# Optimization experiments

Hardware: AMD Instinct MI355X
Metric: run time of the kernel (lower is better)

## Reference

```python
import jax, jax.numpy as jnp
import numpy as np

B, S, D = 4, 4096, 64

def setup_inputs() -> dict:
    key = jax.random.key(0)
    k1, k2, k3 = jax.random.split(key, 3)
    inputs = jax.random.normal(k1, (B, S, D), dtype=jnp.float32)
    rotation = jax.random.normal(k2, (D, D), dtype=jnp.float32)
    entangle = jax.random.normal(k3, (D, D), dtype=jnp.float32)
    return {"inputs": inputs, "rotation": rotation, "entangle": entangle}

def reference(inputs, rotation, entangle):
    # query/key projections: [B,S,D] @ [D,D] -> [B,S,D]
    query = jnp.einsum('bsd,de->bse', inputs, rotation)
    key = jnp.einsum('bsd,de->bse', inputs, entangle)
    scale = 1.0 / jnp.sqrt(jnp.float32(inputs.shape[-1]))
    # scores: [B,S,S] softmax over last axis
    scores = jax.nn.softmax(jnp.einsum('bqd,bkd->bqk', query, key) * scale, axis=-1)
    # values are the raw inputs (no value projection)
    return jnp.einsum('bqk,bkd->bqd', scores, inputs)
```

## Files before the change

kernel.cpp:

```cpp
#include <hip/hip_runtime.h>
#include <hip/hip_fp16.h>

#define BB 4
#define SS 4096
#define DD 64
#define NSPLIT 4
#define KT_PER (SS / 64 / NSPLIT)

typedef _Float16 half8 __attribute__((ext_vector_type(8)));
typedef _Float16 half4 __attribute__((ext_vector_type(4)));
typedef __fp16 fp16x2 __attribute__((ext_vector_type(2)));
typedef float floatx4 __attribute__((ext_vector_type(4)));

__global__ __launch_bounds__(256) void proj_kernel(
    const float* __restrict__ X, const float* __restrict__ R, const float* __restrict__ E,
    _Float16* __restrict__ Qhi, _Float16* __restrict__ Qlo,
    _Float16* __restrict__ Khi, _Float16* __restrict__ Klo,
    _Float16* __restrict__ Vt)
{
    __shared__ float Rs[64][64];
    __shared__ float Es[64][64];
    __shared__ float Xs[16][68];
    int t = threadIdx.x;
    long rowbase = (long)blockIdx.x * 16;

    for (int j = 0; j < 4; ++j) {
        int idx = j * 256 + t;
        int r = idx >> 4;
        int c = (idx & 15) * 4;
        *(float4*)&Rs[r][c] = ((const float4*)R)[idx];
        *(float4*)&Es[r][c] = ((const float4*)E)[idx];
    }
    *(float4*)&Xs[t >> 4][(t & 15) * 4] = ((const float4*)(X + rowbase * 64))[t];
    __syncthreads();

    int row = t >> 4;
    int c0 = (t & 15) * 4;
    float q[4] = {0.f, 0.f, 0.f, 0.f}, k[4] = {0.f, 0.f, 0.f, 0.f};
#pragma unroll 4
    for (int d = 0; d < 64; ++d) {
        float x = Xs[row][d];
        float4 rv = *(const float4*)&Rs[d][c0];
        float4 ev = *(const float4*)&Es[d][c0];
        q[0] = fmaf(x, rv.x, q[0]); q[1] = fmaf(x, rv.y, q[1]);
        q[2] = fmaf(x, rv.z, q[2]); q[3] = fmaf(x, rv.w, q[3]);
        k[0] = fmaf(x, ev.x, k[0]); k[1] = fmaf(x, ev.y, k[1]);
        k[2] = fmaf(x, ev.z, k[2]); k[3] = fmaf(x, ev.w, k[3]);
    }
    long gq = (rowbase + row) * 64 + c0;
    half4 qh, ql, kh, kl;
    for (int j = 0; j < 4; ++j) {
        _Float16 h = (_Float16)q[j];
        qh[j] = h; ql[j] = (_Float16)(q[j] - (float)h);
        h = (_Float16)k[j];
        kh[j] = h; kl[j] = (_Float16)(k[j] - (float)h);
    }
    *(half4*)(Qhi + gq) = qh; *(half4*)(Qlo + gq) = ql;
    *(half4*)(Khi + gq) = kh; *(half4*)(Klo + gq) = kl;

    int d = t >> 2;
    int si = (t & 3) * 4;
    int b = (int)(rowbase >> 12);
    int sbase = (int)(rowbase & 4095);
    half4 v;
    for (int j = 0; j < 4; ++j) v[j] = (_Float16)Xs[si + j][d];
    *(half4*)(Vt + ((long)(b * 64 + d)) * SS + sbase + si) = v;
}

#define L2E 1.44269504088896340736f
#define PD 72

__global__ __launch_bounds__(256, 4) void attn_partial(
    const _Float16* __restrict__ Qhi, const _Float16* __restrict__ Qlo,
    const _Float16* __restrict__ Khi, const _Float16* __restrict__ Klo,
    const _Float16* __restrict__ Vt,
    float* __restrict__ Op, float* __restrict__ Mp, float* __restrict__ Lp)
{
    __shared__ _Float16 Ksh[64][PD];
    __shared__ _Float16 Ksl[64][PD];
    __shared__ _Float16 Vs[64][PD];
    __shared__ _Float16 Ps[4][16][PD];

    int t = threadIdx.x;
    int wave = t >> 6;
    int lane = t & 63;
    int l15 = lane & 15;
    int quad = lane >> 4;
    int split = blockIdx.y;
    int b = blockIdx.z;
    int q0 = blockIdx.x * 64 + wave * 16;

    long qrow = ((long)b * SS + q0 + l15) * DD;
    half8 qa0h = *(const half8*)(Qhi + qrow + quad * 8);
    half8 qa1h = *(const half8*)(Qhi + qrow + 32 + quad * 8);
    half8 qa0l = *(const half8*)(Qlo + qrow + quad * 8);
    half8 qa1l = *(const half8*)(Qlo + qrow + 32 + quad * 8);

    floatx4 o[4];
    for (int i = 0; i < 4; ++i) o[i] = (floatx4){0.f, 0.f, 0.f, 0.f};
    float m_q = -1e30f;
    float l_q = 0.f;

    const float scale = 0.125f * L2E;

    int rr = t >> 2;
    int cc = (t & 3) * 16;
    long kbase = ((long)b * SS + rr) * DD + cc;
    long vbase = ((long)b * 64 + rr) * SS + cc;

    int kt = split * KT_PER;
    uint4 rh0, rh1, rl0, rl1, rv0, rv1;
    {
        const uint4* khsrc = (const uint4*)(Khi + kbase + (long)kt * 64 * DD);
        rh0 = khsrc[0]; rh1 = khsrc[1];
        const uint4* klsrc = (const uint4*)(Klo + kbase + (long)kt * 64 * DD);
        rl0 = klsrc[0]; rl1 = klsrc[1];
        const uint4* vsrc = (const uint4*)(Vt + vbase + kt * 64);
        rv0 = vsrc[0]; rv1 = vsrc[1];
    }

    for (int i = 0; i < KT_PER; ++i) {
        if (i > 0) __syncthreads();
        {
            uint4* khdst = (uint4*)&Ksh[rr][cc];
            khdst[0] = rh0; khdst[1] = rh1;
            uint4* kldst = (uint4*)&Ksl[rr][cc];
            kldst[0] = rl0; kldst[1] = rl1;
            uint4* vdst = (uint4*)&Vs[rr][cc];
            vdst[0] = rv0; vdst[1] = rv1;
        }
        __syncthreads();

        int ktn = (i + 1 < KT_PER) ? (kt + 1) : kt;
        {
            const uint4* khsrc = (const uint4*)(Khi + kbase + (long)ktn * 64 * DD);
            rh0 = khsrc[0]; rh1 = khsrc[1];
            const uint4* klsrc = (const uint4*)(Klo + kbase + (long)ktn * 64 * DD);
            rl0 = klsrc[0]; rl1 = klsrc[1];
            const uint4* vsrc = (const uint4*)(Vt + vbase + ktn * 64);
            rv0 = vsrc[0]; rv1 = vsrc[1];
        }
        kt = ktn;

        floatx4 s[4];
        for (int ct = 0; ct < 4; ++ct) {
            floatx4 acc = {0.f, 0.f, 0.f, 0.f};
            half8 ka0h = *(const half8*)&Ksh[ct * 16 + l15][quad * 8];
            half8 ka1h = *(const half8*)&Ksh[ct * 16 + l15][32 + quad * 8];
            half8 ka0l = *(const half8*)&Ksl[ct * 16 + l15][quad * 8];
            half8 ka1l = *(const half8*)&Ksl[ct * 16 + l15][32 + quad * 8];
            acc = __builtin_amdgcn_mfma_f32_16x16x32_f16(ka0h, qa0h, acc, 0, 0, 0);
            acc = __builtin_amdgcn_mfma_f32_16x16x32_f16(ka1h, qa1h, acc, 0, 0, 0);
            acc = __builtin_amdgcn_mfma_f32_16x16x32_f16(ka0h, qa0l, acc, 0, 0, 0);
            acc = __builtin_amdgcn_mfma_f32_16x16x32_f16(ka1h, qa1l, acc, 0, 0, 0);
            acc = __builtin_amdgcn_mfma_f32_16x16x32_f16(ka0l, qa0h, acc, 0, 0, 0);
            acc = __builtin_amdgcn_mfma_f32_16x16x32_f16(ka1l, qa1h, acc, 0, 0, 0);
            s[ct] = acc;
        }

        float mt = s[0][0];
        for (int ct = 0; ct < 4; ++ct)
            for (int r = 0; r < 4; ++r)
                mt = fmaxf(mt, s[ct][r]);
        mt = fmaxf(mt, __shfl_xor(mt, 16));
        mt = fmaxf(mt, __shfl_xor(mt, 32));
        mt *= scale;
        float mn = fmaxf(m_q, mt);
        float alpha = exp2f(m_q - mn);
        m_q = mn;

        float rs = 0.f;
        for (int ct = 0; ct < 4; ++ct) {
            float p0 = exp2f(s[ct][0] * scale - mn);
            float p1 = exp2f(s[ct][1] * scale - mn);
            float p2 = exp2f(s[ct][2] * scale - mn);
            float p3 = exp2f(s[ct][3] * scale - mn);
            rs += (p0 + p1) + (p2 + p3);
            union { fp16x2 h2[2]; half4 h4; } u;
            u.h2[0] = __builtin_amdgcn_cvt_pkrtz(p0, p1);
            u.h2[1] = __builtin_amdgcn_cvt_pkrtz(p2, p3);
            *(half4*)&Ps[wave][l15][ct * 16 + quad * 4] = u.h4;
        }
        rs += __shfl_xor(rs, 16);
        rs += __shfl_xor(rs, 32);
        l_q = l_q * alpha + rs;

        for (int r = 0; r < 4; ++r) {
            float a = __shfl(alpha, quad * 4 + r);
            o[0][r] *= a; o[1][r] *= a; o[2][r] *= a; o[3][r] *= a;
        }

        for (int h = 0; h < 2; ++h) {
            half8 pa = *(const half8*)&Ps[wave][l15][h * 32 + quad * 8];
            for (int dt = 0; dt < 4; ++dt) {
                half8 vb = *(const half8*)&Vs[dt * 16 + l15][h * 32 + quad * 8];
                o[dt] = __builtin_amdgcn_mfma_f32_16x16x32_f16(pa, vb, o[dt], 0, 0, 0);
            }
        }
    }

    long pbase = ((long)b * NSPLIT + split) * SS;
    for (int r = 0; r < 4; ++r) {
        int q = q0 + quad * 4 + r;
        long orow = (pbase + q) * DD;
        for (int dt = 0; dt < 4; ++dt)
            Op[orow + dt * 16 + l15] = o[dt][r];
    }
    if (quad == 0) {
        Mp[pbase + q0 + l15] = m_q;
        Lp[pbase + q0 + l15] = l_q;
    }
}

__global__ __launch_bounds__(256) void combine_kernel(
    const float* __restrict__ Op, const float* __restrict__ Mp,
    const float* __restrict__ Lp, float* __restrict__ Out)
{
    int t = threadIdx.x;
    int qi = t >> 4;
    int d4 = (t & 15) * 4;
    long gq = (long)blockIdx.x * 16 + qi;
    int b = (int)(gq >> 12);
    int s = (int)(gq & 4095);

    float m = -1e30f;
    for (int i = 0; i < NSPLIT; ++i)
        m = fmaxf(m, Mp[((long)b * NSPLIT + i) * SS + s]);
    float l = 0.f;
    float4 o = {0.f, 0.f, 0.f, 0.f};
    for (int i = 0; i < NSPLIT; ++i) {
        long pb = ((long)b * NSPLIT + i) * SS + s;
        float a = exp2f(Mp[pb] - m);
        l = fmaf(Lp[pb], a, l);
        float4 oi = *(const float4*)(Op + pb * DD + d4);
        o.x = fmaf(oi.x, a, o.x); o.y = fmaf(oi.y, a, o.y);
        o.z = fmaf(oi.z, a, o.z); o.w = fmaf(oi.w, a, o.w);
    }
    float inv = 1.f / l;
    float4 r = {o.x * inv, o.y * inv, o.z * inv, o.w * inv};
    *(float4*)(Out + gq * DD + d4) = r;
}

extern "C" void kernel_launch(void* const* d_in, const int* in_sizes, int n_in,
                              void* d_out, int out_size, void* d_ws, size_t ws_size,
                              hipStream_t stream) {
    const float* X = (const float*)d_in[0];
    const float* R = (const float*)d_in[1];
    const float* E = (const float*)d_in[2];
    float* Out = (float*)d_out;

    const size_t N = (size_t)BB * SS * DD;
    _Float16* Qhi = (_Float16*)d_ws;
    _Float16* Qlo = Qhi + N;
    _Float16* Khi = Qlo + N;
    _Float16* Klo = Khi + N;
    _Float16* Vt  = Klo + N;
    float* Op = (float*)(Vt + N);
    float* Mp = Op + (size_t)BB * NSPLIT * SS * DD;
    float* Lp = Mp + (size_t)BB * NSPLIT * SS;

    proj_kernel<<<dim3(BB * SS / 16), 256, 0, stream>>>(X, R, E, Qhi, Qlo, Khi, Klo, Vt);
    attn_partial<<<dim3(SS / 64, NSPLIT, BB), 256, 0, stream>>>(Qhi, Qlo, Khi, Klo, Vt, Op, Mp, Lp);
    combine_kernel<<<dim3(BB * SS / 16), 256, 0, stream>>>(Op, Mp, Lp, Out);
}
```

Before: 119.8 us.

## Give each attention wave two query tiles and batch projection rows per block

The attention kernel now runs with 128 threads (2 waves), and each wave handles 32 query rows as two 16-row tiles. Each K/V fragment read from shared memory therefore feeds twice as many MFMAs, which cuts LDS traffic per unit of compute. K/V tile loads are redistributed over fewer threads with more loads each. The projection kernel now processes 64 rows per block instead of 16, so the R/E weight loads are amortised over more rows and the Vt stores are wider. Costs are higher register pressure, fewer threads per block, and fewer projection blocks.

```diff
diff --git a/kernel.cpp b/kernel.cpp
--- a/kernel.cpp
+++ b/kernel.cpp
@@ -20,57 +20,69 @@
 {
     __shared__ float Rs[64][64];
     __shared__ float Es[64][64];
-    __shared__ float Xs[16][68];
+    __shared__ float Xs[64][68];
     int t = threadIdx.x;
-    long rowbase = (long)blockIdx.x * 16;
-
+    long rowbase = (long)blockIdx.x * 64;
+
+    const float4* Xg = (const float4*)(X + rowbase * 64);
     for (int j = 0; j < 4; ++j) {
         int idx = j * 256 + t;
         int r = idx >> 4;
         int c = (idx & 15) * 4;
         *(float4*)&Rs[r][c] = ((const float4*)R)[idx];
         *(float4*)&Es[r][c] = ((const float4*)E)[idx];
-    }
-    *(float4*)&Xs[t >> 4][(t & 15) * 4] = ((const float4*)(X + rowbase * 64))[t];
+        *(float4*)&Xs[r][c] = Xg[idx];
+    }
     __syncthreads();
 
-    int row = t >> 4;
+    int rg = t >> 4;
     int c0 = (t & 15) * 4;
-    float q[4] = {0.f, 0.f, 0.f, 0.f}, k[4] = {0.f, 0.f, 0.f, 0.f};
+    float q[4][4], k[4][4];
+    for (int i = 0; i < 4; ++i)
+        for (int j = 0; j < 4; ++j) { q[i][j] = 0.f; k[i][j] = 0.f; }
 #pragma unroll 4
     for (int d = 0; d < 64; ++d) {
-        float x = Xs[row][d];
         float4 rv = *(const float4*)&Rs[d][c0];
         float4 ev = *(const float4*)&Es[d][c0];
-        q[0] = fmaf(x, rv.x, q[0]); q[1] = fmaf(x, rv.y, q[1]);
-        q[2] = fmaf(x, rv.z, q[2]); q[3] = fmaf(x, rv.w, q[3]);
-        k[0] = fmaf(x, ev.x, k[0]); k[1] = fmaf(x, ev.y, k[1]);
-        k[2] = fmaf(x, ev.z, k[2]); k[3] = fmaf(x, ev.w, k[3]);
-    }
-    long gq = (rowbase + row) * 64 + c0;
-    half4 qh, ql, kh, kl;
-    for (int j = 0; j < 4; ++j) {
-        _Float16 h = (_Float16)q[j];
-        qh[j] = h; ql[j] = (_Float16)(q[j] - (float)h);
-        h = (_Float16)k[j];
-        kh[j] = h; kl[j] = (_Float16)(k[j] - (float)h);
-    }
-    *(half4*)(Qhi + gq) = qh; *(half4*)(Qlo + gq) = ql;
-    *(half4*)(Khi + gq) = kh; *(half4*)(Klo + gq) = kl;
+        for (int i = 0; i < 4; ++i) {
+            float x = Xs[rg * 4 + i][d];
+            q[i][0] = fmaf(x, rv.x, q[i][0]); q[i][1] = fmaf(x, rv.y, q[i][1]);
+            q[i][2] = fmaf(x, rv.z, q[i][2]); q[i][3] = fmaf(x, rv.w, q[i][3]);
+            k[i][0] = fmaf(x, ev.x, k[i][0]); k[i][1] = fmaf(x, ev.y, k[i][1]);
+            k[i][2] = fmaf(x, ev.z, k[i][2]); k[i][3] = fmaf(x, ev.w, k[i][3]);
+        }
+    }
+    for (int i = 0; i < 4; ++i) {
+        long gq = (rowbase + rg * 4 + i) * 64 + c0;
+        half4 qh, ql, kh, kl;
+        for (int j = 0; j < 4; ++j) {
+            _Float16 h = (_Float16)q[i][j];
+            qh[j] = h; ql[j] = (_Float16)(q[i][j] - (float)h);
+            h = (_Float16)k[i][j];
+            kh[j] = h; kl[j] = (_Float16)(k[i][j] - (float)h);
+        }
+        *(half4*)(Qhi + gq) = qh; *(half4*)(Qlo + gq) = ql;
+        *(half4*)(Khi + gq) = kh; *(half4*)(Klo + gq) = kl;
+    }
 
     int d = t >> 2;
-    int si = (t & 3) * 4;
+    int si = (t & 3) * 16;
     int b = (int)(rowbase >> 12);
     int sbase = (int)(rowbase & 4095);
-    half4 v;
-    for (int j = 0; j < 4; ++j) v[j] = (_Float16)Xs[si + j][d];
-    *(half4*)(Vt + ((long)(b * 64 + d)) * SS + sbase + si) = v;
+    half8 v0, v1;
+    for (int j = 0; j < 8; ++j) {
+        v0[j] = (_Float16)Xs[si + j][d];
+        v1[j] = (_Float16)Xs[si + 8 + j][d];
+    }
+    _Float16* vp = Vt + ((long)(b * 64 + d)) * SS + sbase + si;
+    *(half8*)vp = v0;
+    *(half8*)(vp + 8) = v1;
 }
 
 #define L2E 1.44269504088896340736f
 #define PD 72
 
-__global__ __launch_bounds__(256, 4) void attn_partial(
+__global__ __launch_bounds__(128, 2) void attn_partial(
     const _Float16* __restrict__ Qhi, const _Float16* __restrict__ Qlo,
     const _Float16* __restrict__ Khi, const _Float16* __restrict__ Klo,
     const _Float16* __restrict__ Vt,
@@ -79,7 +91,7 @@
     __shared__ _Float16 Ksh[64][PD];
     __shared__ _Float16 Ksl[64][PD];
     __shared__ _Float16 Vs[64][PD];
-    __shared__ _Float16 Ps[4][16][PD];
+    __shared__ _Float16 Ps[2][32][PD];
 
     int t = threadIdx.x;
     int wave = t >> 6;
@@ -88,127 +100,144 @@
     int quad = lane >> 4;
     int split = blockIdx.y;
     int b = blockIdx.z;
-    int q0 = blockIdx.x * 64 + wave * 16;
-
-    long qrow = ((long)b * SS + q0 + l15) * DD;
-    half8 qa0h = *(const half8*)(Qhi + qrow + quad * 8);
-    half8 qa1h = *(const half8*)(Qhi + qrow + 32 + quad * 8);
-    half8 qa0l = *(const half8*)(Qlo + qrow + quad * 8);
-    half8 qa1l = *(const half8*)(Qlo + qrow + 32 + quad * 8);
-
-    floatx4 o[4];
-    for (int i = 0; i < 4; ++i) o[i] = (floatx4){0.f, 0.f, 0.f, 0.f};
-    float m_q = -1e30f;
-    float l_q = 0.f;
+    int q0 = blockIdx.x * 64 + wave * 32;
+
+    half8 qah[2][2], qal[2][2];
+    for (int qh = 0; qh < 2; ++qh) {
+        long qrow = ((long)b * SS + q0 + qh * 16 + l15) * DD;
+        qah[qh][0] = *(const half8*)(Qhi + qrow + quad * 8);
+        qah[qh][1] = *(const half8*)(Qhi + qrow + 32 + quad * 8);
+        qal[qh][0] = *(const half8*)(Qlo + qrow + quad * 8);
+        qal[qh][1] = *(const half8*)(Qlo + qrow + 32 + quad * 8);
+    }
+
+    floatx4 o[2][4];
+    for (int qh = 0; qh < 2; ++qh)
+        for (int i = 0; i < 4; ++i) o[qh][i] = (floatx4){0.f, 0.f, 0.f, 0.f};
+    float m_q[2] = {-1e30f, -1e30f};
+    float l_q[2] = {0.f, 0.f};
 
     const float scale = 0.125f * L2E;
 
-    int rr = t >> 2;
-    int cc = (t & 3) * 16;
-    long kbase = ((long)b * SS + rr) * DD + cc;
-    long vbase = ((long)b * 64 + rr) * SS + cc;
-
+    int erow = t >> 3;
+    int eel = (t & 7) * 8;
+    long ktilebase = ((long)b * SS) * DD;
     int kt = split * KT_PER;
-    uint4 rh0, rh1, rl0, rl1, rv0, rv1;
+
+    uint4 rh[4], rl[4], rv[4];
     {
-        const uint4* khsrc = (const uint4*)(Khi + kbase + (long)kt * 64 * DD);
-        rh0 = khsrc[0]; rh1 = khsrc[1];
-        const uint4* klsrc = (const uint4*)(Klo + kbase + (long)kt * 64 * DD);
-        rl0 = klsrc[0]; rl1 = klsrc[1];
-        const uint4* vsrc = (const uint4*)(Vt + vbase + kt * 64);
-        rv0 = vsrc[0]; rv1 = vsrc[1];
+        const uint4* khsrc = (const uint4*)(Khi + ktilebase + (long)kt * 64 * DD) + t;
+        const uint4* klsrc = (const uint4*)(Klo + ktilebase + (long)kt * 64 * DD) + t;
+        for (int j = 0; j < 4; ++j) {
+            rh[j] = khsrc[j * 128];
+            rl[j] = klsrc[j * 128];
+            int d = j * 16 + erow;
+            rv[j] = *(const uint4*)(Vt + ((long)(b * 64 + d)) * SS + kt * 64 + eel);
+        }
     }
 
     for (int i = 0; i < KT_PER; ++i) {
         if (i > 0) __syncthreads();
-        {
-            uint4* khdst = (uint4*)&Ksh[rr][cc];
-            khdst[0] = rh0; khdst[1] = rh1;
-            uint4* kldst = (uint4*)&Ksl[rr][cc];
-            kldst[0] = rl0; kldst[1] = rl1;
-            uint4* vdst = (uint4*)&Vs[rr][cc];
-            vdst[0] = rv0; vdst[1] = rv1;
+        for (int j = 0; j < 4; ++j) {
+            int rr = j * 16 + erow;
+            *(uint4*)&Ksh[rr][eel] = rh[j];
+            *(uint4*)&Ksl[rr][eel] = rl[j];
+            *(uint4*)&Vs[rr][eel] = rv[j];
         }
         __syncthreads();
 
         int ktn = (i + 1 < KT_PER) ? (kt + 1) : kt;
         {
-            const uint4* khsrc = (const uint4*)(Khi + kbase + (long)ktn * 64 * DD);
-            rh0 = khsrc[0]; rh1 = khsrc[1];
-            const uint4* klsrc = (const uint4*)(Klo + kbase + (long)ktn * 64 * DD);
-            rl0 = klsrc[0]; rl1 = klsrc[1];
-            const uint4* vsrc = (const uint4*)(Vt + vbase + ktn * 64);
-            rv0 = vsrc[0]; rv1 = vsrc[1];
+            const uint4* khsrc = (const uint4*)(Khi + ktilebase + (long)ktn * 64 * DD) + t;
+            const uint4* klsrc = (const uint4*)(Klo + ktilebase + (long)ktn * 64 * DD) + t;
+            for (int j = 0; j < 4; ++j) {
+                rh[j] = khsrc[j * 128];
+                rl[j] = klsrc[j * 128];
+                int d = j * 16 + erow;
+                rv[j] = *(const uint4*)(Vt + ((long)(b * 64 + d)) * SS + ktn * 64 + eel);
+            }
         }
         kt = ktn;
 
-        floatx4 s[4];
+        floatx4 s[2][4];
         for (int ct = 0; ct < 4; ++ct) {
-            floatx4 acc = {0.f, 0.f, 0.f, 0.f};
             half8 ka0h = *(const half8*)&Ksh[ct * 16 + l15][quad * 8];
             half8 ka1h = *(const half8*)&Ksh[ct * 16 + l15][32 + quad * 8];
             half8 ka0l = *(const half8*)&Ksl[ct * 16 + l15][quad * 8];
             half8 ka1l = *(const half8*)&Ksl[ct * 16 + l15][32 + quad * 8];
-            acc = __builtin_amdgcn_mfma_f32_16x16x32_f16(ka0h, qa0h, acc, 0, 0, 0);
-            acc = __builtin_amdgcn_mfma_f32_16x16x32_f16(ka1h, qa1h, acc, 0, 0, 0);
-            acc = __builtin_amdgcn_mfma_f32_16x16x32_f16(ka0h, qa0l, acc, 0, 0, 0);
-            acc = __builtin_amdgcn_mfma_f32_16x16x32_f16(ka1h, qa1l, acc, 0, 0, 0);
-            acc = __builtin_amdgcn_mfma_f32_16x16x32_f16(ka0l, qa0h, acc, 0, 0, 0);
-            acc = __builtin_amdgcn_mfma_f32_16x16x32_f16(ka1l, qa1h, acc, 0, 0, 0);
-            s[ct] = acc;
-        }
-
-        float mt = s[0][0];
-        for (int ct = 0; ct < 4; ++ct)
-            for (int r = 0; r < 4; ++r)
-                mt = fmaxf(mt, s[ct][r]);
-        mt = fmaxf(mt, __shfl_xor(mt, 16));
-        mt = fmaxf(mt, __shfl_xor(mt, 32));
-        mt *= scale;
-        float mn = fmaxf(m_q, mt);
-        float alpha = exp2f(m_q - mn);
-        m_q = mn;
-
-        float rs = 0.f;
-        for (int ct = 0; ct < 4; ++ct) {
-            float p0 = exp2f(s[ct][0] * scale - mn);
-            float p1 = exp2f(s[ct][1] * scale - mn);
-            float p2 = exp2f(s[ct][2] * scale - mn);
-            float p3 = exp2f(s[ct][3] * scale - mn);
-            rs += (p0 + p1) + (p2 + p3);
-            union { fp16x2 h2[2]; half4 h4; } u;
-            u.h2[0] = __builtin_amdgcn_cvt_pkrtz(p0, p1);
-            u.h2[1] = __builtin_amdgcn_cvt_pkrtz(p2, p3);
-            *(half4*)&Ps[wave][l15][ct * 16 + quad * 4] = u.h4;
-        }
-        rs += __shfl_xor(rs, 16);
-        rs += __shfl_xor(rs, 32);
-        l_q = l_q * alpha + rs;
-
-        for (int r = 0; r < 4; ++r) {
-            float a = __shfl(alpha, quad * 4 + r);
-            o[0][r] *= a; o[1][r] *= a; o[2][r] *= a; o[3][r] *= a;
+            for (int qh = 0; qh < 2; ++qh) {
+                floatx4 acc = {0.f, 0.f, 0.f, 0.f};
+                acc = __builtin_amdgcn_mfma_f32_16x16x32_f16(ka0h, qah[qh][0], acc, 0, 0, 0);
+                acc = __builtin_amdgcn_mfma_f32_16x16x32_f16(ka1h, qah[qh][1], acc, 0, 0, 0);
+                acc = __builtin_amdgcn_mfma_f32_16x16x32_f16(ka0h, qal[qh][0], acc, 0, 0, 0);
+                acc = __builtin_amdgcn_mfma_f32_16x16x32_f16(ka1h, qal[qh][1], acc, 0, 0, 0);
+                acc = __builtin_amdgcn_mfma_f32_16x16x32_f16(ka0l, qah[qh][0], acc, 0, 0, 0);
+                acc = __builtin_amdgcn_mfma_f32_16x16x32_f16(ka1l, qah[qh][1], acc, 0, 0, 0);
+                s[qh][ct] = acc;
+            }
+        }
+
+        float alpha[2];
+        for (int qh = 0; qh < 2; ++qh) {
+            float mt = s[qh][0][0];
+            for (int ct = 0; ct < 4; ++ct)
+                for (int r = 0; r < 4; ++r)
+                    mt = fmaxf(mt, s[qh][ct][r]);
+            mt = fmaxf(mt, __shfl_xor(mt, 16));
+            mt = fmaxf(mt, __shfl_xor(mt, 32));
+            mt *= scale;
+            float mn = fmaxf(m_q[qh], mt);
+            alpha[qh] = exp2f(m_q[qh] - mn);
+            m_q[qh] = mn;
+
+            float rs = 0.f;
+            for (int ct = 0; ct < 4; ++ct) {
+                float p0 = exp2f(s[qh][ct][0] * scale - mn);
+                float p1 = exp2f(s[qh][ct][1] * scale - mn);
+                float p2 = exp2f(s[qh][ct][2] * scale - mn);
+                float p3 = exp2f(s[qh][ct][3] * scale - mn);
+                rs += (p0 + p1) + (p2 + p3);
+                union { fp16x2 h2[2]; half4 h4; } u;
+                u.h2[0] = __builtin_amdgcn_cvt_pkrtz(p0, p1);
+                u.h2[1] = __builtin_amdgcn_cvt_pkrtz(p2, p3);
+                *(half4*)&Ps[wave][qh * 16 + l15][ct * 16 + quad * 4] = u.h4;
+            }
+            rs += __shfl_xor(rs, 16);
+            rs += __shfl_xor(rs, 32);
+            l_q[qh] = l_q[qh] * alpha[qh] + rs;
+
+            for (int r = 0; r < 4; ++r) {
+                float a = __shfl(alpha[qh], quad * 4 + r);
+                o[qh][0][r] *= a; o[qh][1][r] *= a;
+                o[qh][2][r] *= a; o[qh][3][r] *= a;
+            }
         }
 
         for (int h = 0; h < 2; ++h) {
-            half8 pa = *(const half8*)&Ps[wave][l15][h * 32 + quad * 8];
+            half8 pa0 = *(const half8*)&Ps[wave][l15][h * 32 + quad * 8];
+            half8 pa1 = *(const half8*)&Ps[wave][16 + l15][h * 32 + quad * 8];
             for (int dt = 0; dt < 4; ++dt) {
                 half8 vb = *(const half8*)&Vs[dt * 16 + l15][h * 32 + quad * 8];
-                o[dt] = __builtin_amdgcn_mfma_f32_16x16x32_f16(pa, vb, o[dt], 0, 0, 0);
+                o[0][dt] = __builtin_amdgcn_mfma_f32_16x16x32_f16(pa0, vb, o[0][dt], 0, 0, 0);
+                o[1][dt] = __builtin_amdgcn_mfma_f32_16x16x32_f16(pa1, vb, o[1][dt], 0, 0, 0);
             }
         }
     }
 
     long pbase = ((long)b * NSPLIT + split) * SS;
-    for (int r = 0; r < 4; ++r) {
-        int q = q0 + quad * 4 + r;
-        long orow = (pbase + q) * DD;
-        for (int dt = 0; dt < 4; ++dt)
-            Op[orow + dt * 16 + l15] = o[dt][r];
+    for (int qh = 0; qh < 2; ++qh) {
+        for (int r = 0; r < 4; ++r) {
+            int q = q0 + qh * 16 + quad * 4 + r;
+            long orow = (pbase + q) * DD;
+            for (int dt = 0; dt < 4; ++dt)
+                Op[orow + dt * 16 + l15] = o[qh][dt][r];
+        }
     }
     if (quad == 0) {
-        Mp[pbase + q0 + l15] = m_q;
-        Lp[pbase + q0 + l15] = l_q;
+        for (int qh = 0; qh < 2; ++qh) {
+            Mp[pbase + q0 + qh * 16 + l15] = m_q[qh];
+            Lp[pbase + q0 + qh * 16 + l15] = l_q[qh];
+        }
     }
 }
 
@@ -259,7 +288,7 @@
     float* Mp = Op + (size_t)BB * NSPLIT * SS * DD;
     float* Lp = Mp + (size_t)BB * NSPLIT * SS;
 
-    proj_kernel<<<dim3(BB * SS / 16), 256, 0, stream>>>(X, R, E, Qhi, Qlo, Khi, Klo, Vt);
-    attn_partial<<<dim3(SS / 64, NSPLIT, BB), 256, 0, stream>>>(Qhi, Qlo, Khi, Klo, Vt, Op, Mp, Lp);
+    proj_kernel<<<dim3(BB * SS / 64), 256, 0, stream>>>(X, R, E, Qhi, Qlo, Khi, Klo, Vt);
+    attn_partial<<<dim3(SS / 64, NSPLIT, BB), 128, 0, stream>>>(Qhi, Qlo, Khi, Klo, Vt, Op, Mp, Lp);
     combine_kernel<<<dim3(BB * SS / 16), 256, 0, stream>>>(Op, Mp, Lp, Out);
 }
```

After: 218.1 us. 1.82x slower.

## Use 2-wave blocks with 32 queries per wave and direct global-to-LDS loads

Applied to the files above, without the earlier changes.

The attention kernel now runs 128-thread blocks in which each wave handles 32 query rows (two 16-row MFMA groups), so every K/V fragment read from LDS is reused across twice as many queries. K and V tiles are copied with global_load_lds into XOR-swizzled, unpadded LDS buffers instead of being staged through registers. The register-prefetch double buffer is removed, so global loads are no longer overlapped with compute. Register pressure per wave also rises.

```diff
diff --git a/kernel.cpp b/kernel.cpp
--- a/kernel.cpp
+++ b/kernel.cpp
@@ -49,6 +49,7 @@
     }
     long gq = (rowbase + row) * 64 + c0;
     half4 qh, ql, kh, kl;
+#pragma unroll
     for (int j = 0; j < 4; ++j) {
         _Float16 h = (_Float16)q[j];
         qh[j] = h; ql[j] = (_Float16)(q[j] - (float)h);
@@ -63,23 +64,29 @@
     int b = (int)(rowbase >> 12);
     int sbase = (int)(rowbase & 4095);
     half4 v;
+#pragma unroll
     for (int j = 0; j < 4; ++j) v[j] = (_Float16)Xs[si + j][d];
     *(half4*)(Vt + ((long)(b * 64 + d)) * SS + sbase + si) = v;
 }
 
 #define L2E 1.44269504088896340736f
-#define PD 72
-
-__global__ __launch_bounds__(256, 4) void attn_partial(
+
+__device__ __forceinline__ void glds16(const _Float16* g, _Float16* l) {
+    __builtin_amdgcn_global_load_lds(
+        (const __attribute__((address_space(1))) unsigned*)g,
+        (__attribute__((address_space(3))) unsigned*)l, 16, 0, 0);
+}
+
+__global__ __launch_bounds__(128, 2) void attn_partial(
     const _Float16* __restrict__ Qhi, const _Float16* __restrict__ Qlo,
     const _Float16* __restrict__ Khi, const _Float16* __restrict__ Klo,
     const _Float16* __restrict__ Vt,
     float* __restrict__ Op, float* __restrict__ Mp, float* __restrict__ Lp)
 {
-    __shared__ _Float16 Ksh[64][PD];
-    __shared__ _Float16 Ksl[64][PD];
-    __shared__ _Float16 Vs[64][PD];
-    __shared__ _Float16 Ps[4][16][PD];
+    __shared__ _Float16 Ksh[64 * 64];
+    __shared__ _Float16 Ksl[64 * 64];
+    __shared__ _Float16 Vs[64 * 64];
+    __shared__ _Float16 Ps[2][32][72];
 
     int t = threadIdx.x;
     int wave = t >> 6;
@@ -88,127 +95,154 @@
     int quad = lane >> 4;
     int split = blockIdx.y;
     int b = blockIdx.z;
-    int q0 = blockIdx.x * 64 + wave * 16;
-
-    long qrow = ((long)b * SS + q0 + l15) * DD;
-    half8 qa0h = *(const half8*)(Qhi + qrow + quad * 8);
-    half8 qa1h = *(const half8*)(Qhi + qrow + 32 + quad * 8);
-    half8 qa0l = *(const half8*)(Qlo + qrow + quad * 8);
-    half8 qa1l = *(const half8*)(Qlo + qrow + 32 + quad * 8);
-
-    floatx4 o[4];
-    for (int i = 0; i < 4; ++i) o[i] = (floatx4){0.f, 0.f, 0.f, 0.f};
-    float m_q = -1e30f;
-    float l_q = 0.f;
+    int q0 = blockIdx.x * 64 + wave * 32;
+
+    half8 qah0, qah1, qbh0, qbh1, qal0, qal1, qbl0, qbl1;
+    {
+        long qrow = ((long)b * SS + q0 + l15) * DD;
+        qah0 = *(const half8*)(Qhi + qrow + quad * 8);
+        qah1 = *(const half8*)(Qhi + qrow + 32 + quad * 8);
+        qal0 = *(const half8*)(Qlo + qrow + quad * 8);
+        qal1 = *(const half8*)(Qlo + qrow + 32 + quad * 8);
+        long qrow2 = qrow + 16 * DD;
+        qbh0 = *(const half8*)(Qhi + qrow2 + quad * 8);
+        qbh1 = *(const half8*)(Qhi + qrow2 + 32 + quad * 8);
+        qbl0 = *(const half8*)(Qlo + qrow2 + quad * 8);
+        qbl1 = *(const half8*)(Qlo + qrow2 + 32 + quad * 8);
+    }
+
+    floatx4 o[2][4];
+#pragma unroll
+    for (int qh = 0; qh < 2; ++qh)
+#pragma unroll
+        for (int i = 0; i < 4; ++i) o[qh][i] = (floatx4){0.f, 0.f, 0.f, 0.f};
+    float m_q[2] = {-1e30f, -1e30f};
+    float l_q[2] = {0.f, 0.f};
 
     const float scale = 0.125f * L2E;
 
-    int rr = t >> 2;
-    int cc = (t & 3) * 16;
-    long kbase = ((long)b * SS + rr) * DD + cc;
-    long vbase = ((long)b * 64 + rr) * SS + cc;
+    int grow = lane >> 3;
+    int gblk = (lane & 7) ^ grow;
+    int rm = l15 & 7;
+    int p0h = ((quad ^ rm) << 3);
 
     int kt = split * KT_PER;
-    uint4 rh0, rh1, rl0, rl1, rv0, rv1;
-    {
-        const uint4* khsrc = (const uint4*)(Khi + kbase + (long)kt * 64 * DD);
-        rh0 = khsrc[0]; rh1 = khsrc[1];
-        const uint4* klsrc = (const uint4*)(Klo + kbase + (long)kt * 64 * DD);
-        rl0 = klsrc[0]; rl1 = klsrc[1];
-        const uint4* vsrc = (const uint4*)(Vt + vbase + kt * 64);
-        rv0 = vsrc[0]; rv1 = vsrc[1];
-    }
-
-    for (int i = 0; i < KT_PER; ++i) {
-        if (i > 0) __syncthreads();
+    for (int i = 0; i < KT_PER; ++i, ++kt) {
+        __syncthreads();
         {
-            uint4* khdst = (uint4*)&Ksh[rr][cc];
-            khdst[0] = rh0; khdst[1] = rh1;
-            uint4* kldst = (uint4*)&Ksl[rr][cc];
-            kldst[0] = rl0; kldst[1] = rl1;
-            uint4* vdst = (uint4*)&Vs[rr][cc];
-            vdst[0] = rv0; vdst[1] = rv1;
+            long ktile = ((long)b * SS + (long)kt * 64) * DD;
+            const _Float16* khs = Khi + ktile;
+            const _Float16* kls = Klo + ktile;
+            const _Float16* vtb = Vt + (long)b * 64 * SS + kt * 64;
+#pragma unroll
+            for (int j = 0; j < 4; ++j) {
+                int c = wave * 4 + j;
+                int row = c * 8 + grow;
+                long goff = (long)row * 64 + gblk * 8;
+                glds16(khs + goff, &Ksh[c * 512]);
+                glds16(kls + goff, &Ksl[c * 512]);
+                glds16(vtb + (long)row * SS + gblk * 8, &Vs[c * 512]);
+            }
         }
         __syncthreads();
 
-        int ktn = (i + 1 < KT_PER) ? (kt + 1) : kt;
-        {
-            const uint4* khsrc = (const uint4*)(Khi + kbase + (long)ktn * 64 * DD);
-            rh0 = khsrc[0]; rh1 = khsrc[1];
-            const uint4* klsrc = (const uint4*)(Klo + kbase + (long)ktn * 64 * DD);
-            rl0 = klsrc[0]; rl1 = klsrc[1];
-            const uint4* vsrc = (const uint4*)(Vt + vbase + ktn * 64);
-            rv0 = vsrc[0]; rv1 = vsrc[1];
-        }
-        kt = ktn;
-
-        floatx4 s[4];
+        floatx4 s[2][4];
+#pragma unroll
         for (int ct = 0; ct < 4; ++ct) {
-            floatx4 acc = {0.f, 0.f, 0.f, 0.f};
-            half8 ka0h = *(const half8*)&Ksh[ct * 16 + l15][quad * 8];
-            half8 ka1h = *(const half8*)&Ksh[ct * 16 + l15][32 + quad * 8];
-            half8 ka0l = *(const half8*)&Ksl[ct * 16 + l15][quad * 8];
-            half8 ka1l = *(const half8*)&Ksl[ct * 16 + l15][32 + quad * 8];
-            acc = __builtin_amdgcn_mfma_f32_16x16x32_f16(ka0h, qa0h, acc, 0, 0, 0);
-            acc = __builtin_amdgcn_mfma_f32_16x16x32_f16(ka1h, qa1h, acc, 0, 0, 0);
-            acc = __builtin_amdgcn_mfma_f32_16x16x32_f16(ka0h, qa0l, acc, 0, 0, 0);
-            acc = __builtin_amdgcn_mfma_f32_16x16x32_f16(ka1h, qa1l, acc, 0, 0, 0);
-            acc = __builtin_amdgcn_mfma_f32_16x16x32_f16(ka0l, qa0h, acc, 0, 0, 0);
-            acc = __builtin_amdgcn_mfma_f32_16x16x32_f16(ka1l, qa1h, acc, 0, 0, 0);
-            s[ct] = acc;
-        }
-
-        float mt = s[0][0];
-        for (int ct = 0; ct < 4; ++ct)
-            for (int r = 0; r < 4; ++r)
-                mt = fmaxf(mt, s[ct][r]);
-        mt = fmaxf(mt, __shfl_xor(mt, 16));
-        mt = fmaxf(mt, __shfl_xor(mt, 32));
-        mt *= scale;
-        float mn = fmaxf(m_q, mt);
-        float alpha = exp2f(m_q - mn);
-        m_q = mn;
-
-        float rs = 0.f;
-        for (int ct = 0; ct < 4; ++ct) {
-            float p0 = exp2f(s[ct][0] * scale - mn);
-            float p1 = exp2f(s[ct][1] * scale - mn);
-            float p2 = exp2f(s[ct][2] * scale - mn);
-            float p3 = exp2f(s[ct][3] * scale - mn);
-            rs += (p0 + p1) + (p2 + p3);
-            union { fp16x2 h2[2]; half4 h4; } u;
-            u.h2[0] = __builtin_amdgcn_cvt_pkrtz(p0, p1);
-            u.h2[1] = __builtin_amdgcn_cvt_pkrtz(p2, p3);
-            *(half4*)&Ps[wave][l15][ct * 16 + quad * 4] = u.h4;
-        }
-        rs += __shfl_xor(rs, 16);
-        rs += __shfl_xor(rs, 32);
-        l_q = l_q * alpha + rs;
-
+            int rowb = (ct * 16 + l15) * 64;
+            half8 ka0h = *(const half8*)&Ksh[rowb + p0h];
+            half8 ka1h = *(const half8*)&Ksh[rowb + (p0h ^ 32)];
+            half8 ka0l = *(const half8*)&Ksl[rowb + p0h];
+            half8 ka1l = *(const half8*)&Ksl[rowb + (p0h ^ 32)];
+            floatx4 acc0 = {0.f, 0.f, 0.f, 0.f};
+            acc0 = __builtin_amdgcn_mfma_f32_16x16x32_f16(ka0h, qah0, acc0, 0, 0, 0);
+            acc0 = __builtin_amdgcn_mfma_f32_16x16x32_f16(ka1h, qah1, acc0, 0, 0, 0);
+            acc0 = __builtin_amdgcn_mfma_f32_16x16x32_f16(ka0h, qal0, acc0, 0, 0, 0);
+            acc0 = __builtin_amdgcn_mfma_f32_16x16x32_f16(ka1h, qal1, acc0, 0, 0, 0);
+            acc0 = __builtin_amdgcn_mfma_f32_16x16x32_f16(ka0l, qah0, acc0, 0, 0, 0);
+            acc0 = __builtin_amdgcn_mfma_f32_16x16x32_f16(ka1l, qah1, acc0, 0, 0, 0);
+            s[0][ct] = acc0;
+            floatx4 acc1 = {0.f, 0.f, 0.f, 0.f};
+            acc1 = __builtin_amdgcn_mfma_f32_16x16x32_f16(ka0h, qbh0, acc1, 0, 0, 0);
+            acc1 = __builtin_amdgcn_mfma_f32_16x16x32_f16(ka1h, qbh1, acc1, 0, 0, 0);
+            acc1 = __builtin_amdgcn_mfma_f32_16x16x32_f16(ka0h, qbl0, acc1, 0, 0, 0);
+            acc1 = __builtin_amdgcn_mfma_f32_16x16x32_f16(ka1h, qbl1, acc1, 0, 0, 0);
+            acc1 = __builtin_amdgcn_mfma_f32_16x16x32_f16(ka0l, qbh0, acc1, 0, 0, 0);
+            acc1 = __builtin_amdgcn_mfma_f32_16x16x32_f16(ka1l, qbh1, acc1, 0, 0, 0);
+            s[1][ct] = acc1;
+        }
+
+#pragma unroll
+        for (int qh = 0; qh < 2; ++qh) {
+            float mt = s[qh][0][0];
+#pragma unroll
+            for (int ct = 0; ct < 4; ++ct)
+#pragma unroll
+                for (int r = 0; r < 4; ++r)
+                    mt = fmaxf(mt, s[qh][ct][r]);
+            mt = fmaxf(mt, __shfl_xor(mt, 16));
+            mt = fmaxf(mt, __shfl_xor(mt, 32));
+            mt *= scale;
+            float mn = fmaxf(m_q[qh], mt);
+            float alpha = exp2f(m_q[qh] - mn);
+            m_q[qh] = mn;
+
+            float rs = 0.f;
+#pragma unroll
+            for (int ct = 0; ct < 4; ++ct) {
+                float p0 = exp2f(s[qh][ct][0] * scale - mn);
+                float p1 = exp2f(s[qh][ct][1] * scale - mn);
+                float p2 = exp2f(s[qh][ct][2] * scale - mn);
+                float p3 = exp2f(s[qh][ct][3] * scale - mn);
+                rs += (p0 + p1) + (p2 + p3);
+                union { fp16x2 h2[2]; half4 h4; } u;
+                u.h2[0] = __builtin_amdgcn_cvt_pkrtz(p0, p1);
+                u.h2[1] = __builtin_amdgcn_cvt_pkrtz(p2, p3);
+                *(half4*)&Ps[wave][qh * 16 + l15][ct * 16 + quad * 4] = u.h4;
+            }
+            rs += __shfl_xor(rs, 16);
+            rs += __shfl_xor(rs, 32);
+            l_q[qh] = l_q[qh] * alpha + rs;
+
+#pragma unroll
+            for (int r = 0; r < 4; ++r) {
+                float a = __shfl(alpha, quad * 4 + r);
+                o[qh][0][r] *= a; o[qh][1][r] *= a;
+                o[qh][2][r] *= a; o[qh][3][r] *= a;
+            }
+        }
+
+#pragma unroll
+        for (int h = 0; h < 2; ++h) {
+            half8 pa0 = *(const half8*)&Ps[wave][l15][h * 32 + quad * 8];
+            half8 pa1 = *(const half8*)&Ps[wave][16 + l15][h * 32 + quad * 8];
+#pragma unroll
+            for (int dt = 0; dt < 4; ++dt) {
+                int rowb = (dt * 16 + l15) * 64;
+                half8 vb = *(const half8*)&Vs[rowb + (p0h ^ (h << 5))];
+                o[0][dt] = __builtin_amdgcn_mfma_f32_16x16x32_f16(pa0, vb, o[0][dt], 0, 0, 0);
+                o[1][dt] = __builtin_amdgcn_mfma_f32_16x16x32_f16(pa1, vb, o[1][dt], 0, 0, 0);
+            }
+        }
+    }
+
+    long pbase = ((long)b * NSPLIT + split) * SS;
+#pragma unroll
+    for (int qh = 0; qh < 2; ++qh) {
+#pragma unroll
         for (int r = 0; r < 4; ++r) {
-            float a = __shfl(alpha, quad * 4 + r);
-            o[0][r] *= a; o[1][r] *= a; o[2][r] *= a; o[3][r] *= a;
-        }
-
-        for (int h = 0; h < 2; ++h) {
-            half8 pa = *(const half8*)&Ps[wave][l15][h * 32 + quad * 8];
-            for (int dt = 0; dt < 4; ++dt) {
-                half8 vb = *(const half8*)&Vs[dt * 16 + l15][h * 32 + quad * 8];
-                o[dt] = __builtin_amdgcn_mfma_f32_16x16x32_f16(pa, vb, o[dt], 0, 0, 0);
-            }
-        }
-    }
-
-    long pbase = ((long)b * NSPLIT + split) * SS;
-    for (int r = 0; r < 4; ++r) {
-        int q = q0 + quad * 4 + r;
-        long orow = (pbase + q) * DD;
-        for (int dt = 0; dt < 4; ++dt)
-            Op[orow + dt * 16 + l15] = o[dt][r];
+            int q = q0 + qh * 16 + quad * 4 + r;
+            long orow = (pbase + q) * DD;
+#pragma unroll
+            for (int dt = 0; dt < 4; ++dt)
+                Op[orow + dt * 16 + l15] = o[qh][dt][r];
+        }
     }
     if (quad == 0) {
-        Mp[pbase + q0 + l15] = m_q;
-        Lp[pbase + q0 + l15] = l_q;
+        Mp[pbase + q0 + l15] = m_q[0];
+        Lp[pbase + q0 + l15] = l_q[0];
+        Mp[pbase + q0 + 16 + l15] = m_q[1];
+        Lp[pbase + q0 + 16 + l15] = l_q[1];
     }
 }
 
@@ -260,6 +294,6 @@
     float* Lp = Mp + (size_t)BB * NSPLIT * SS;
 
     proj_kernel<<<dim3(BB * SS / 16), 256, 0, stream>>>(X, R, E, Qhi, Qlo, Khi, Klo, Vt);
-    attn_partial<<<dim3(SS / 64, NSPLIT, BB), 256, 0, stream>>>(Qhi, Qlo, Khi, Klo, Vt, Op, Mp, Lp);
+    attn_partial<<<dim3(SS / 64, NSPLIT, BB), 128, 0, stream>>>(Qhi, Qlo, Khi, Klo, Vt, Op, Mp, Lp);
     combine_kernel<<<dim3(BB * SS / 16), 256, 0, stream>>>(Op, Mp, Lp, Out);
 }
```

Result: slower. 123.5 us (+3.0%).
